# Optimization experiments

Measured on AMD Instinct MI355X. Metric: run time of the kernel, lower is better.

Reference implementation:

```python
import jax, jax.numpy as jnp
import numpy as np

HIDDEN = 256
TOPK = 16
SINK_BLOCKS = 5
TAU = 1.0
SOFT_ALPHA = 8.0
LN_EPS = 1e-5


def setup_inputs() -> dict:
    key = jax.random.key(0)
    ks = jax.random.split(key, 8)
    B, T, QD, KD, J = 2, 1024, 1024, 1024, 64
    H = HIDDEN
    H3 = 3 * H
    s = 0.02
    return {
        "Q": jax.random.normal(ks[0], (B, T, QD), dtype=jnp.float32),
        "K": jax.random.normal(ks[1], (B, J, KD), dtype=jnp.float32),
        "Wq": jax.random.normal(ks[2], (H, QD), dtype=jnp.float32) * s,
        "Wk": jax.random.normal(ks[3], (H, KD), dtype=jnp.float32) * s,
        "ln_g": jnp.ones((H3,), dtype=jnp.float32),
        "ln_b": jnp.zeros((H3,), dtype=jnp.float32),
        "Wu": jax.random.normal(ks[4], (H, H3), dtype=jnp.float32) * s,
        "bu": jnp.zeros((H,), dtype=jnp.float32),
        "Wv": jax.random.normal(ks[5], (H, H3), dtype=jnp.float32) * s,
        "bv": jnp.zeros((H,), dtype=jnp.float32),
        "Wo": jax.random.normal(ks[6], (1, H), dtype=jnp.float32) * s,
        "bo": jnp.zeros((1,), dtype=jnp.float32),
        "chunk_len": 16,
        "L_ctx": 1024,
    }


def _forward(Q, K, Wq, Wk, ln_g, ln_b, Wu, bu, Wv, bv, Wo, bo, chunk_len, L_ctx):
    B, T, _ = Q.shape
    J = K.shape[1]
    # ---- GatedScorer ----
    q = jnp.einsum('btd,hd->bth', Q, Wq)  # (B,T,H)
    k = jnp.einsum('bjd,hd->bjh', K, Wk)  # (B,J,H)
    H = q.shape[-1]
    qb = jnp.broadcast_to(q[:, :, None, :], (B, T, J, H))
    kb = jnp.broadcast_to(k[:, None, :, :], (B, T, J, H))
    x = jnp.concatenate([qb, kb, qb * kb], axis=-1)  # (B,T,J,3H)
    mu = jnp.mean(x, axis=-1, keepdims=True)
    var = jnp.mean((x - mu) ** 2, axis=-1, keepdims=True)
    x = (x - mu) / jnp.sqrt(var + LN_EPS) * ln_g + ln_b
    U = jnp.einsum('btjc,hc->btjh', x, Wu) + bu
    V = jnp.einsum('btjc,hc->btjh', x, Wv) + bv
    Z = U * jax.nn.gelu(V, approximate=False)
    logits = jnp.einsum('btjh,oh->btjo', Z, Wo)[..., 0] + bo[0]  # (B,T,J)

    # ---- top-k chunk selection (deterministic path, use_learnable_k=False) ----
    sink = int(min(max(0, SINK_BLOCKS), J))
    J_tail = J - sink
    topk_main = max(min(J, TOPK) - sink, 0)
    logits_tail = logits[..., sink:]  # (B,T,J_tail)
    causal = jnp.arange(J_tail)[None, :] <= jnp.arange(T)[:, None]  # tril(T,J_tail)
    masked = jnp.where(causal[None], logits_tail, -jnp.inf)
    _, idx_tail = jax.lax.top_k(masked, topk_main)
    idx_tail = idx_tail + sink
    sink_idx = jnp.broadcast_to(jnp.arange(sink)[None, None, :], (B, T, sink))
    idx = jnp.concatenate([sink_idx, idx_tail], axis=-1)  # (B,T,sink+topk_main)

    # ---- soft warmup weights ----
    w_soft = jax.nn.softmax(logits / TAU, axis=-1)  # (B,T,J)

    # ---- build_block_bias_from_topk ----
    num_chunks = (L_ctx + chunk_len - 1) // chunk_len
    sel = jnp.zeros((B, T, num_chunks), dtype=bool)
    sel = sel.at[jnp.arange(B)[:, None, None], jnp.arange(T)[None, :, None], idx].set(True)
    token_chunk = jnp.clip(jnp.arange(L_ctx) // chunk_len, 0, num_chunks - 1)  # (L_ctx,)
    sel_tok = jnp.take(sel, token_chunk, axis=-1)  # (B,T,L_ctx)
    per_chunk_bias = -SOFT_ALPHA * (1.0 - w_soft)  # (B,T,J)
    bias = jnp.take(per_chunk_bias, token_chunk, axis=-1)  # (B,T,L_ctx)
    bias = jnp.where(sel_tok, 0.0, bias)
    tri = jnp.arange(L_ctx)[None, :] > jnp.arange(T)[:, None]  # triu(T,L_ctx, diag=1)
    bias = jnp.where(tri[None], -jnp.inf, bias)
    return logits, bias


def reference(Q, K, Wq, Wk, ln_g, ln_b, Wu, bu, Wv, bv, Wo, bo, chunk_len, L_ctx):
    return _forward(Q, K, Wq, Wk, ln_g, ln_b, Wu, bu, Wv, bv, Wo, bo, chunk_len, L_ctx)
```

## Files before the change

kernel.cpp:

```cpp
#include <hip/hip_runtime.h>
#include <hip/hip_bf16.h>
#include <math.h>

#define H3 768

#define OFF_Q     0u
#define OFF_K     524288u
#define OFF_UVK   557056u
#define OFF_SQ    622592u
#define OFF_SQ2   624768u
#define OFF_WGU   626944u
#define OFF_WGV   627200u
#define OFF_CU    627456u
#define OFF_CV    627712u
#define OFF_Q2    627968u
#define OFF_K2    1152256u

#define BO_UVQ   0u
#define BO_WQF   1048576u
#define BO_WKF   1310720u
#define BO_BPK   1572864u
#define BO_WQBF  1703936u
#define BO_WKBF  1835008u

typedef __attribute__((ext_vector_type(8))) short bf16x8;
typedef __attribute__((ext_vector_type(4))) float f32x4;

__device__ __forceinline__ float bf2f(short s) {
    return __uint_as_float(((unsigned)(unsigned short)s) << 16);
}
union bfu { __hip_bfloat162 h; short2 s; };
__device__ __forceinline__ void split2(float a, float b, short* hi2, short* lo2) {
    bfu h; h.h = __float22bfloat162_rn(float2{a, b});
    float fa = bf2f(h.s.x), fb = bf2f(h.s.y);
    bfu l; l.h = __float22bfloat162_rn(float2{a - fa, b - fb});
    hi2[0] = h.s.x; hi2[1] = h.s.y;
    lo2[0] = l.s.x; lo2[1] = l.s.y;
}
__device__ __forceinline__ void split8(const float* v, bf16x8* vh, bf16x8* vl) {
    short h2[2], l2[2];
#pragma unroll
    for (int i = 0; i < 4; i++) {
        split2(v[2 * i], v[2 * i + 1], h2, l2);
        (*vh)[2 * i] = h2[0]; (*vh)[2 * i + 1] = h2[1];
        (*vl)[2 * i] = l2[0]; (*vl)[2 * i + 1] = l2[1];
    }
}

__device__ __forceinline__ float gelu_fast(float v) {
    float ar = v * 0.70710678118654752440f;
    float a = fabsf(ar);
    float t = __builtin_amdgcn_rcpf(fmaf(0.3275911f, a, 1.0f));
    float p = fmaf(fmaf(fmaf(fmaf(1.061405429f, t, -1.453152027f), t,
                             1.421413741f), t, -0.284496736f), t, 0.254829592f) * t;
    float e = __expf(-ar * ar);
    float er = fmaf(-p, e, 1.0f);
    er = copysignf(er, ar);
    return 0.5f * v * (1.0f + er);
}

__device__ __forceinline__ float wave_reduce_add(float v) {
#pragma unroll
    for (int off = 32; off > 0; off >>= 1) v += __shfl_xor(v, off, 64);
    return v;
}

__global__ __launch_bounds__(256) void prep(const float* __restrict__ Wq,
                                            const float* __restrict__ Wk,
                                            const float* __restrict__ Wu,
                                            const float* __restrict__ Wv,
                                            const float* __restrict__ g,
                                            const float* __restrict__ lb,
                                            const float* __restrict__ bu,
                                            const float* __restrict__ bv,
                                            float* __restrict__ ws,
                                            float* __restrict__ bsc) {
    int tid = threadIdx.x;
    int bid = blockIdx.x;
    if (bid < 64) {
        int h = bid * 4 + (tid >> 6);
        int lane = tid & 63;
        float su = 0.f, sv = 0.f, tu = 0.f, tv = 0.f;
#pragma unroll
        for (int i = 0; i < 12; i++) {
            int c = lane + 64 * i;
            float gg = g[c], bb = lb[c];
            float wu = Wu[h * H3 + c], wv = Wv[h * H3 + c];
            su += wu * gg; sv += wv * gg; tu += wu * bb; tv += wv * bb;
        }
        su = wave_reduce_add(su); sv = wave_reduce_add(sv);
        tu = wave_reduce_add(tu); tv = wave_reduce_add(tv);
        if (lane == 0) {
            ws[OFF_WGU + h] = su; ws[OFF_WGV + h] = sv;
            ws[OFF_CU + h] = tu + bu[h]; ws[OFF_CV + h] = tv + bv[h];
        }
        return;
    }
    float v8[8];
    bf16x8 vh, vl;
    if (bid < 320) {
        const float* W; bf16x8* dst;
        int idx;
        if (bid < 192) { idx = (bid - 64) * 256 + tid; W = Wq; dst = (bf16x8*)(bsc + BO_WQF); }
        else { idx = (bid - 192) * 256 + tid; W = Wk; dst = (bf16x8*)(bsc + BO_WKF); }
        int n = idx >> 7, k8 = idx & 127;
        const float* src = W + (size_t)n * 1024 + k8 * 8;
        *(float4*)&v8[0] = *(const float4*)src;
        *(float4*)&v8[4] = *(const float4*)(src + 4);
        split8(v8, &vh, &vl);
        int kc = k8 >> 2, grp = k8 & 3, lane = grp * 16 + (n & 15), ntg = n >> 4;
        size_t s0 = ((size_t)(kc * 16 + ntg) * 2) * 64 + lane;
        dst[s0] = vh; dst[s0 + 64] = vl;
        return;
    }
    int idx, c0;
    bf16x8* dst;
    int n;
    if (bid < 384) {
        idx = (bid - 320) * 256 + tid;
        n = idx >> 5; c0 = (idx & 31) * 8;
        dst = (bf16x8*)(bsc + BO_WQBF);
    } else if (bid < 448) {
        idx = (bid - 384) * 256 + tid;
        n = idx >> 5; c0 = 256 + (idx & 31) * 8;
        dst = (bf16x8*)(bsc + BO_WKBF);
    } else {
        idx = (bid - 448) * 256 + tid;
        n = idx >> 5; c0 = 512 + (idx & 31) * 8;
        dst = (bf16x8*)(bsc + BO_BPK);
    }
    int h, uv;
    if (bid < 448) { uv = (n < 256) ? 0 : 1; h = (n < 256) ? n : n - 256; }
    else {
        int ntg0 = n >> 4, cc = n & 15;
        uv = ntg0 & 1;
        h = ((ntg0 >> 3) << 6) | (((ntg0 >> 1) & 3) << 4) | cc;
    }
    const float* W = uv ? Wv : Wu;
#pragma unroll
    for (int i = 0; i < 8; i++) v8[i] = W[(size_t)h * H3 + c0 + i] * g[c0 + i];
    split8(v8, &vh, &vl);
    int k8 = (c0 & 255) >> 3;
    int kc = k8 >> 2, grp = k8 & 3, lane = grp * 16 + (n & 15), ntg = n >> 4;
    size_t s0 = ((size_t)(kc * 32 + ntg) * 2) * 64 + lane;
    dst[s0] = vh; dst[s0 + 64] = vl;
}

__global__ __launch_bounds__(256) void proj_mfma(const float* __restrict__ Q,
                                                 const float* __restrict__ Kin,
                                                 const float* __restrict__ bsc,
                                                 float* __restrict__ ws) {
    __shared__ __align__(16) short Ah[2][32 * 40], Al[2][32 * 40];
    int tid = threadIdx.x, bx = blockIdx.x, by = blockIdx.y, ks = blockIdx.z;
    const float* A; float* C; const bf16x8* BF;
    if (by < 64) {
        A = Q + (size_t)by * 32 * 1024;
        C = ws + (ks ? OFF_Q2 : OFF_Q) + (size_t)by * 32 * 256;
        BF = (const bf16x8*)(bsc + BO_WQF);
    } else {
        A = Kin + (size_t)(by - 64) * 32 * 1024;
        C = ws + (ks ? OFF_K2 : OFF_K) + (size_t)(by - 64) * 32 * 256;
        BF = (const bf16x8*)(bsc + BO_WKF);
    }
    int w = tid >> 6, l = tid & 63, c15 = l & 15, grp = l >> 4;
    int mt = w & 1, np = w >> 1;
    int srow = tid >> 3, scol = (tid & 7) * 4;
    const float* arow = A + (size_t)srow * 1024 + ks * 512 + scol;
    f32x4 acc[2];
    acc[0] = (f32x4){0.f, 0.f, 0.f, 0.f};
    acc[1] = (f32x4){0.f, 0.f, 0.f, 0.f};
    float4 a4 = *(const float4*)&arow[0];
    for (int kc = 0; kc < 16; kc++) {
        int pb = kc & 1;
        short h4[4], l4[4];
        split2(a4.x, a4.y, &h4[0], &l4[0]);
        split2(a4.z, a4.w, &h4[2], &l4[2]);
        int ao = srow * 40 + scol;
        *(short4*)&Ah[pb][ao] = *(short4*)&h4[0];
        *(short4*)&Al[pb][ao] = *(short4*)&l4[0];
        if (kc < 15) a4 = *(const float4*)&arow[(kc + 1) * 32];
        __syncthreads();
        int fo = (mt * 16 + c15) * 40 + grp * 8;
        bf16x8 afh = *(const bf16x8*)&Ah[pb][fo];
        bf16x8 afl = *(const bf16x8*)&Al[pb][fo];
        int kcg = ks * 16 + kc;
        bf16x8 bh[2], bl[2];
#pragma unroll
        for (int i = 0; i < 2; i++) {
            int ntg = bx * 4 + 2 * np + i;
            size_t fi = ((size_t)(kcg * 16 + ntg) * 2) * 64 + l;
            bh[i] = BF[fi]; bl[i] = BF[fi + 64];
        }
#pragma unroll
        for (int i = 0; i < 2; i++)
            acc[i] = __builtin_amdgcn_mfma_f32_16x16x32_bf16(afl, bh[i], acc[i], 0, 0, 0);
#pragma unroll
        for (int i = 0; i < 2; i++)
            acc[i] = __builtin_amdgcn_mfma_f32_16x16x32_bf16(afh, bl[i], acc[i], 0, 0, 0);
#pragma unroll
        for (int i = 0; i < 2; i++)
            acc[i] = __builtin_amdgcn_mfma_f32_16x16x32_bf16(afh, bh[i], acc[i], 0, 0, 0);
    }
#pragma unroll
    for (int r = 0; r < 4; r++) {
        int rloc = mt * 16 + grp * 4 + r;
#pragma unroll
        for (int i = 0; i < 2; i++)
            C[(size_t)rloc * 256 + bx * 64 + (2 * np + i) * 16 + c15] = acc[i][r];
    }
}

__global__ __launch_bounds__(256) void uv_mfma(float* __restrict__ ws,
                                               float* __restrict__ bsc) {
    __shared__ __align__(16) short Ah[64 * 40], Al[64 * 40];
    int tid = threadIdx.x, bx = blockIdx.x, by = blockIdx.y;
    const float* A1; const float* A2; float* C; const bf16x8* BF; int sbase;
    if (by < 32) {
        A1 = ws + OFF_Q + (size_t)by * 64 * 256;
        A2 = ws + OFF_Q2 + (size_t)by * 64 * 256;
        C = bsc + BO_UVQ + (size_t)by * 64 * 512;
        BF = (const bf16x8*)(bsc + BO_WQBF);
        sbase = by * 64;
    } else {
        A1 = ws + OFF_K + (size_t)(by - 32) * 64 * 256;
        A2 = ws + OFF_K2 + (size_t)(by - 32) * 64 * 256;
        C = ws + OFF_UVK + (size_t)(by - 32) * 64 * 512;
        BF = (const bf16x8*)(bsc + BO_WKBF);
        sbase = 2048 + (by - 32) * 64;
    }
    int w = tid >> 6, l = tid & 63, c15 = l & 15, grp = l >> 4;
    int srow = tid >> 2, scol = (tid & 3) * 8;
    f32x4 acc[4];
#pragma unroll
    for (int nt = 0; nt < 4; nt++) acc[nt] = (f32x4){0.f, 0.f, 0.f, 0.f};
    float s1 = 0.f, s2 = 0.f;
    for (int kc = 0; kc < 8; kc++) {
        float v8[8], u8[8];
        const float* src1 = &A1[(size_t)srow * 256 + kc * 32 + scol];
        const float* src2 = &A2[(size_t)srow * 256 + kc * 32 + scol];
        *(float4*)&v8[0] = *(const float4*)src1;
        *(float4*)&v8[4] = *(const float4*)(src1 + 4);
        *(float4*)&u8[0] = *(const float4*)src2;
        *(float4*)&u8[4] = *(const float4*)(src2 + 4);
#pragma unroll
        for (int i = 0; i < 8; i++) v8[i] += u8[i];
        if (bx == 0) {
#pragma unroll
            for (int i = 0; i < 8; i++) { s1 += v8[i]; s2 = fmaf(v8[i], v8[i], s2); }
        }
        bf16x8 vh, vl;
        split8(v8, &vh, &vl);
        int ao = srow * 40 + scol;
        *(bf16x8*)&Ah[ao] = vh;
        *(bf16x8*)&Al[ao] = vl;
        __syncthreads();
        int fo = (w * 16 + c15) * 40 + grp * 8;
        bf16x8 afh = *(const bf16x8*)&Ah[fo];
        bf16x8 afl = *(const bf16x8*)&Al[fo];
        bf16x8 bh[4], bl[4];
#pragma unroll
        for (int nt = 0; nt < 4; nt++) {
            int ntg = bx * 4 + nt;
            size_t fi = ((size_t)(kc * 32 + ntg) * 2) * 64 + l;
            bh[nt] = BF[fi]; bl[nt] = BF[fi + 64];
        }
#pragma unroll
        for (int nt = 0; nt < 4; nt++)
            acc[nt] = __builtin_amdgcn_mfma_f32_16x16x32_bf16(afl, bh[nt], acc[nt], 0, 0, 0);
#pragma unroll
        for (int nt = 0; nt < 4; nt++)
            acc[nt] = __builtin_amdgcn_mfma_f32_16x16x32_bf16(afh, bl[nt], acc[nt], 0, 0, 0);
#pragma unroll
        for (int nt = 0; nt < 4; nt++)
            acc[nt] = __builtin_amdgcn_mfma_f32_16x16x32_bf16(afh, bh[nt], acc[nt], 0, 0, 0);
        __syncthreads();
    }
    if (bx == 0) {
        s1 += __shfl_xor(s1, 1, 64); s1 += __shfl_xor(s1, 2, 64);
        s2 += __shfl_xor(s2, 1, 64); s2 += __shfl_xor(s2, 2, 64);
        if ((tid & 3) == 0) {
            ws[OFF_SQ + sbase + srow] = s1;
            ws[OFF_SQ2 + sbase + srow] = s2;
        }
    }
#pragma unroll
    for (int nt = 0; nt < 4; nt++)
#pragma unroll
        for (int r = 0; r < 4; r++)
            C[(size_t)(w * 16 + grp * 4 + r) * 512 + bx * 64 + nt * 16 + c15] = acc[nt][r];
}

__global__ __launch_bounds__(256, 2) void main_mfma(const float* __restrict__ ws,
                                                    const float* __restrict__ bsc,
                                                    const float* __restrict__ Wo,
                                                    const float* __restrict__ bo,
                                                    float* __restrict__ logits) {
    __shared__ float kk[256];
    __shared__ __align__(16) short Ah[8][64 * 32];
    __shared__ __align__(16) short Al[8][64 * 32];
    __shared__ float mu_s[64], inv_s[64];
    __shared__ float part_s[4][64];
    int tid = threadIdx.x;
    int bidf = blockIdx.x;
    int ti = ((bidf & 7) << 1) | ((bidf >> 3) & 1);
    int j = (bidf >> 4) & 63;
    int b = bidf >> 10;
    int t0 = ti << 6;
    int bj = (b << 6) | j;
    int rot8 = bidf & 7;
    kk[tid] = ws[OFF_K + bj * 256 + tid] + ws[OFF_K2 + bj * 256 + tid];
    int w = tid >> 6, l = tid & 63, c15 = l & 15, grp = l >> 4;
    int srow = tid >> 2, scol = (tid & 3) * 8;
    const float* qrow = ws + OFF_Q + (size_t)((b << 10) + t0 + srow) * 256 + scol;
    const float* q2row = ws + OFF_Q2 + (size_t)((b << 10) + t0 + srow) * 256 + scol;
    const bf16x8* bpk = (const bf16x8*)(bsc + BO_BPK);
    const float* UVQ = bsc + BO_UVQ;
    f32x4 acc[4][8];
#pragma unroll
    for (int mt = 0; mt < 4; mt++)
#pragma unroll
        for (int nt = 0; nt < 8; nt++) acc[mt][nt] = (f32x4){0.f, 0.f, 0.f, 0.f};
    float s1 = 0.f, s2 = 0.f;
    int ntg0 = w * 8;
    __syncthreads();
#pragma unroll
    for (int kc = 0; kc < 8; kc++) {
        float q8[8], p8[8], kv[8];
        *(float4*)&q8[0] = *(const float4*)&qrow[kc * 32];
        *(float4*)&q8[4] = *(const float4*)&qrow[kc * 32 + 4];
        *(float4*)&p8[0] = *(const float4*)&q2row[kc * 32];
        *(float4*)&p8[4] = *(const float4*)&q2row[kc * 32 + 4];
        *(float4*)&kv[0] = *(const float4*)&kk[kc * 32 + scol];
        *(float4*)&kv[4] = *(const float4*)&kk[kc * 32 + scol + 4];
        bf16x8 vh, vl;
        short htmp[2], ltmp[2];
#pragma unroll
        for (int i = 0; i < 4; i++) {
            float a = (q8[2 * i] + p8[2 * i]) * kv[2 * i];
            float c = (q8[2 * i + 1] + p8[2 * i + 1]) * kv[2 * i + 1];
            s1 += a + c;
            s2 = fmaf(a, a, s2); s2 = fmaf(c, c, s2);
            split2(a, c, htmp, ltmp);
            vh[2 * i] = htmp[0]; vh[2 * i + 1] = htmp[1];
            vl[2 * i] = ltmp[0]; vl[2 * i + 1] = ltmp[1];
        }
        int ao = srow * 32 + scol;
        *(bf16x8*)&Ah[kc][ao] = vh;
        *(bf16x8*)&Al[kc][ao] = vl;
    }
    s1 += __shfl_xor(s1, 1, 64); s1 += __shfl_xor(s1, 2, 64);
    s2 += __shfl_xor(s2, 1, 64); s2 += __shfl_xor(s2, 2, 64);
    if ((tid & 3) == 0) {
        int row = (b << 10) + t0 + srow;
        float sq = s1 + ws[OFF_SQ + row] + ws[OFF_SQ + 2048 + bj];
        float sq2 = s2 + ws[OFF_SQ2 + row] + ws[OFF_SQ2 + 2048 + bj];
        float muv = sq * (1.0f / 768.0f);
        float ex2 = sq2 * (1.0f / 768.0f);
        mu_s[srow] = muv;
        inv_s[srow] = 1.0f / sqrtf(ex2 - muv * muv + 1e-5f);
    }
    __syncthreads();
#pragma unroll
    for (int ii = 0; ii < 8; ii++) {
        int kcg = (ii + rot8) & 7;
        bf16x8 afh[4], afl[4];
#pragma unroll
        for (int mt = 0; mt < 4; mt++) {
            int ao = (mt * 16 + c15) * 32 + grp * 8;
            afh[mt] = *(const bf16x8*)&Ah[kcg][ao];
            afl[mt] = *(const bf16x8*)&Al[kcg][ao];
        }
        const bf16x8* bpc = bpk + ((size_t)(kcg * 32 + ntg0) * 2) * 64 + l;
#pragma unroll
        for (int nt = 0; nt < 8; nt++) {
            bf16x8 bh = bpc[(size_t)nt * 128];
            bf16x8 bl = bpc[(size_t)nt * 128 + 64];
#pragma unroll
            for (int mt = 0; mt < 4; mt++)
                acc[mt][nt] = __builtin_amdgcn_mfma_f32_16x16x32_bf16(afl[mt], bh, acc[mt][nt], 0, 0, 0);
#pragma unroll
            for (int mt = 0; mt < 4; mt++)
                acc[mt][nt] = __builtin_amdgcn_mfma_f32_16x16x32_bf16(afh[mt], bl, acc[mt][nt], 0, 0, 0);
#pragma unroll
            for (int mt = 0; mt < 4; mt++)
                acc[mt][nt] = __builtin_amdgcn_mfma_f32_16x16x32_bf16(afh[mt], bh, acc[mt][nt], 0, 0, 0);
        }
    }
    float wgu_r[4], wgv_r[4], cu_r[4], cv_r[4], wo_r[4], uk_r[4], vk_r[4];
    int h4[4];
#pragma unroll
    for (int a = 0; a < 4; a++) {
        int h = (w << 6) | (a << 4) | c15;
        h4[a] = h;
        wgu_r[a] = ws[OFF_WGU + h]; wgv_r[a] = ws[OFF_WGV + h];
        cu_r[a] = ws[OFF_CU + h]; cv_r[a] = ws[OFF_CV + h];
        wo_r[a] = Wo[h];
        uk_r[a] = ws[OFF_UVK + (size_t)bj * 512 + h];
        vk_r[a] = ws[OFF_UVK + (size_t)bj * 512 + 256 + h];
    }
#pragma unroll
    for (int mt = 0; mt < 4; mt++) {
#pragma unroll
        for (int r4 = 0; r4 < 4; r4++) {
            int r = mt * 16 + grp * 4 + r4;
            int row = (b << 10) + t0 + r;
            float muv = mu_s[r], invv = inv_s[r];
            const float* uvq = UVQ + (size_t)row * 512;
            float part = 0.f;
#pragma unroll
            for (int a = 0; a < 4; a++) {
                float U = invv * (acc[mt][2 * a][r4] + uvq[h4[a]] + uk_r[a] - muv * wgu_r[a]) + cu_r[a];
                float V = invv * (acc[mt][2 * a + 1][r4] + uvq[256 + h4[a]] + vk_r[a] - muv * wgv_r[a]) + cv_r[a];
                part = fmaf(wo_r[a] * U, gelu_fast(V), part);
            }
            part += __shfl_xor(part, 1, 64);
            part += __shfl_xor(part, 2, 64);
            part += __shfl_xor(part, 4, 64);
            part += __shfl_xor(part, 8, 64);
            if (c15 == 0) part_s[w][r] = part;
        }
    }
    __syncthreads();
    if (tid < 64) {
        float v = bo[0] + part_s[0][tid] + part_s[1][tid] + part_s[2][tid] + part_s[3][tid];
        logits[(size_t)((b << 10) + t0 + tid) * 64 + j] = v;
    }
}

__global__ __launch_bounds__(256) void topk_bias(const float* __restrict__ logits,
                                                 float* __restrict__ bias,
                                                 const int* __restrict__ p_cl,
                                                 const int* __restrict__ p_L) {
    int wv = threadIdx.x >> 6, lane = threadIdx.x & 63;
    int row = blockIdx.x * 4 + wv;
    int t = row & 1023;
    __shared__ float pcb[4][64];
    float L = logits[(size_t)row * 64 + lane];
    float mx = L;
#pragma unroll
    for (int off = 32; off > 0; off >>= 1) mx = fmaxf(mx, __shfl_xor(mx, off, 64));
    float e = expf(L - mx);
    float s = wave_reduce_add(e);
    pcb[wv][lane] = -8.0f * (1.0f - e / s);
    bool valid = (lane >= 5) && ((lane - 5) <= t);
    float val = (lane >= 5) ? (valid ? L : -INFINITY) : -INFINITY;
    int idv = (lane >= 5) ? lane : (1 << 28);
    unsigned long long selmask = 0x1Full;
    for (int it = 0; it < 11; it++) {
        float bv = val; int bi = idv;
#pragma unroll
        for (int off = 32; off > 0; off >>= 1) {
            float ov = __shfl_xor(bv, off, 64);
            int oi = __shfl_xor(bi, off, 64);
            if (ov > bv || (ov == bv && oi < bi)) { bv = ov; bi = oi; }
        }
        selmask |= 1ull << bi;
        if (lane == bi) { val = -INFINITY; idv = (1 << 27); }
    }
    int clen = p_cl[0], Lctx = p_L[0];
    int nch1 = (Lctx + clen - 1) / clen - 1;
    float* brow = bias + (size_t)row * Lctx;
    if ((Lctx & 3) == 0) {
        float4* brow4 = (float4*)brow;
        for (int q = lane; q < (Lctx >> 2); q += 64) {
            float o[4];
#pragma unroll
            for (int i = 0; i < 4; i++) {
                int ll = 4 * q + i;
                int c = min(min((unsigned)ll / (unsigned)clen, (unsigned)nch1), 63u);
                float v;
                if (ll > t) v = -1e30f;
                else if ((selmask >> c) & 1ull) v = 0.0f;
                else v = pcb[wv][c];
                o[i] = v;
            }
            brow4[q] = *(float4*)&o[0];
        }
    } else {
        for (int ll = lane; ll < Lctx; ll += 64) {
            int c = min(min((unsigned)ll / (unsigned)clen, (unsigned)nch1), 63u);
            float v;
            if (ll > t) v = -1e30f;
            else if ((selmask >> c) & 1ull) v = 0.0f;
            else v = pcb[wv][c];
            brow[ll] = v;
        }
    }
}

extern "C" void kernel_launch(void* const* d_in, const int* in_sizes, int n_in,
                              void* d_out, int out_size, void* d_ws, size_t ws_size,
                              hipStream_t stream) {
    const float* Q   = (const float*)d_in[0];
    const float* Kin = (const float*)d_in[1];
    const float* Wq  = (const float*)d_in[2];
    const float* Wk  = (const float*)d_in[3];
    const float* g   = (const float*)d_in[4];
    const float* lb  = (const float*)d_in[5];
    const float* Wu  = (const float*)d_in[6];
    const float* bu  = (const float*)d_in[7];
    const float* Wv  = (const float*)d_in[8];
    const float* bv  = (const float*)d_in[9];
    const float* Wo  = (const float*)d_in[10];
    const float* bo  = (const float*)d_in[11];
    const int* p_cl  = (const int*)d_in[12];
    const int* p_L   = (const int*)d_in[13];
    float* ws = (float*)d_ws;
    float* logits = (float*)d_out;
    float* bias = (float*)d_out + (size_t)2 * 1024 * 64;

    prep<<<512, 256, 0, stream>>>(Wq, Wk, Wu, Wv, g, lb, bu, bv, ws, bias);
    proj_mfma<<<dim3(4, 68, 2), 256, 0, stream>>>(Q, Kin, bias, ws);
    uv_mfma<<<dim3(8, 34), 256, 0, stream>>>(ws, bias);
    main_mfma<<<2048, 256, 0, stream>>>(ws, bias, Wo, bo, logits);
    topk_bias<<<512, 256, 0, stream>>>(logits, bias, p_cl, p_L);
}
```

Measured before the change: 234.1 us.

## Enlarge main_mfma tile to 128 rows with 512-thread blocks

```diff
diff --git a/kernel.cpp b/kernel.cpp
--- a/kernel.cpp
+++ b/kernel.cpp
@@ -290,38 +290,38 @@
             C[(size_t)(w * 16 + grp * 4 + r) * 512 + bx * 64 + nt * 16 + c15] = acc[nt][r];
 }
 
-__global__ __launch_bounds__(256, 2) void main_mfma(const float* __restrict__ ws,
+__global__ __launch_bounds__(512, 2) void main_mfma(const float* __restrict__ ws,
                                                     const float* __restrict__ bsc,
                                                     const float* __restrict__ Wo,
                                                     const float* __restrict__ bo,
                                                     float* __restrict__ logits) {
     __shared__ float kk[256];
-    __shared__ __align__(16) short Ah[8][64 * 32];
-    __shared__ __align__(16) short Al[8][64 * 32];
-    __shared__ float mu_s[64], inv_s[64];
-    __shared__ float part_s[4][64];
+    __shared__ __align__(16) short Ah[8][128 * 32];
+    __shared__ __align__(16) short Al[8][128 * 32];
+    __shared__ float mu_s[128], inv_s[128];
+    __shared__ float part_s[8][128];
     int tid = threadIdx.x;
     int bidf = blockIdx.x;
-    int ti = ((bidf & 7) << 1) | ((bidf >> 3) & 1);
-    int j = (bidf >> 4) & 63;
-    int b = bidf >> 10;
-    int t0 = ti << 6;
+    int ti = bidf & 7;
+    int j = (bidf >> 3) & 63;
+    int b = bidf >> 9;
+    int t0 = ti << 7;
     int bj = (b << 6) | j;
-    int rot8 = bidf & 7;
-    kk[tid] = ws[OFF_K + bj * 256 + tid] + ws[OFF_K2 + bj * 256 + tid];
+    int rot8 = (bidf >> 3) & 7;
+    if (tid < 256) kk[tid] = ws[OFF_K + bj * 256 + tid] + ws[OFF_K2 + bj * 256 + tid];
     int w = tid >> 6, l = tid & 63, c15 = l & 15, grp = l >> 4;
     int srow = tid >> 2, scol = (tid & 3) * 8;
     const float* qrow = ws + OFF_Q + (size_t)((b << 10) + t0 + srow) * 256 + scol;
     const float* q2row = ws + OFF_Q2 + (size_t)((b << 10) + t0 + srow) * 256 + scol;
     const bf16x8* bpk = (const bf16x8*)(bsc + BO_BPK);
     const float* UVQ = bsc + BO_UVQ;
-    f32x4 acc[4][8];
-#pragma unroll
-    for (int mt = 0; mt < 4; mt++)
-#pragma unroll
-        for (int nt = 0; nt < 8; nt++) acc[mt][nt] = (f32x4){0.f, 0.f, 0.f, 0.f};
+    f32x4 acc[8][4];
+#pragma unroll
+    for (int mt = 0; mt < 8; mt++)
+#pragma unroll
+        for (int nt = 0; nt < 4; nt++) acc[mt][nt] = (f32x4){0.f, 0.f, 0.f, 0.f};
     float s1 = 0.f, s2 = 0.f;
-    int ntg0 = w * 8;
+    int ntg0 = w * 4;
     __syncthreads();
 #pragma unroll
     for (int kc = 0; kc < 8; kc++) {
@@ -363,35 +363,43 @@
 #pragma unroll
     for (int ii = 0; ii < 8; ii++) {
         int kcg = (ii + rot8) & 7;
-        bf16x8 afh[4], afl[4];
-#pragma unroll
-        for (int mt = 0; mt < 4; mt++) {
-            int ao = (mt * 16 + c15) * 32 + grp * 8;
-            afh[mt] = *(const bf16x8*)&Ah[kcg][ao];
-            afl[mt] = *(const bf16x8*)&Al[kcg][ao];
-        }
+        bf16x8 bh[4], bl[4];
         const bf16x8* bpc = bpk + ((size_t)(kcg * 32 + ntg0) * 2) * 64 + l;
 #pragma unroll
-        for (int nt = 0; nt < 8; nt++) {
-            bf16x8 bh = bpc[(size_t)nt * 128];
-            bf16x8 bl = bpc[(size_t)nt * 128 + 64];
-#pragma unroll
-            for (int mt = 0; mt < 4; mt++)
-                acc[mt][nt] = __builtin_amdgcn_mfma_f32_16x16x32_bf16(afl[mt], bh, acc[mt][nt], 0, 0, 0);
-#pragma unroll
-            for (int mt = 0; mt < 4; mt++)
-                acc[mt][nt] = __builtin_amdgcn_mfma_f32_16x16x32_bf16(afh[mt], bl, acc[mt][nt], 0, 0, 0);
-#pragma unroll
-            for (int mt = 0; mt < 4; mt++)
-                acc[mt][nt] = __builtin_amdgcn_mfma_f32_16x16x32_bf16(afh[mt], bh, acc[mt][nt], 0, 0, 0);
-        }
-    }
-    float wgu_r[4], wgv_r[4], cu_r[4], cv_r[4], wo_r[4], uk_r[4], vk_r[4];
-    int h4[4];
-#pragma unroll
-    for (int a = 0; a < 4; a++) {
-        int h = (w << 6) | (a << 4) | c15;
-        h4[a] = h;
+        for (int nt = 0; nt < 4; nt++) {
+            bh[nt] = bpc[(size_t)nt * 128];
+            bl[nt] = bpc[(size_t)nt * 128 + 64];
+        }
+#pragma unroll
+        for (int half = 0; half < 2; half++) {
+            bf16x8 afh[4], afl[4];
+#pragma unroll
+            for (int m4 = 0; m4 < 4; m4++) {
+                int ao = ((half * 4 + m4) * 16 + c15) * 32 + grp * 8;
+                afh[m4] = *(const bf16x8*)&Ah[kcg][ao];
+                afl[m4] = *(const bf16x8*)&Al[kcg][ao];
+            }
+#pragma unroll
+            for (int nt = 0; nt < 4; nt++) {
+#pragma unroll
+                for (int m4 = 0; m4 < 4; m4++)
+                    acc[half * 4 + m4][nt] = __builtin_amdgcn_mfma_f32_16x16x32_bf16(afl[m4], bh[nt], acc[half * 4 + m4][nt], 0, 0, 0);
+#pragma unroll
+                for (int m4 = 0; m4 < 4; m4++)
+                    acc[half * 4 + m4][nt] = __builtin_amdgcn_mfma_f32_16x16x32_bf16(afh[m4], bl[nt], acc[half * 4 + m4][nt], 0, 0, 0);
+#pragma unroll
+                for (int m4 = 0; m4 < 4; m4++)
+                    acc[half * 4 + m4][nt] = __builtin_amdgcn_mfma_f32_16x16x32_bf16(afh[m4], bh[nt], acc[half * 4 + m4][nt], 0, 0, 0);
+            }
+        }
+    }
+    float wgu_r[2], wgv_r[2], cu_r[2], cv_r[2], wo_r[2], uk_r[2], vk_r[2];
+    int h2[2];
+#pragma unroll
+    for (int a = 0; a < 2; a++) {
+        int ntg = 4 * w + 2 * a;
+        int h = ((ntg >> 3) << 6) | (((ntg >> 1) & 3) << 4) | c15;
+        h2[a] = h;
         wgu_r[a] = ws[OFF_WGU + h]; wgv_r[a] = ws[OFF_WGV + h];
         cu_r[a] = ws[OFF_CU + h]; cv_r[a] = ws[OFF_CV + h];
         wo_r[a] = Wo[h];
@@ -399,7 +407,7 @@
         vk_r[a] = ws[OFF_UVK + (size_t)bj * 512 + 256 + h];
     }
 #pragma unroll
-    for (int mt = 0; mt < 4; mt++) {
+    for (int mt = 0; mt < 8; mt++) {
 #pragma unroll
         for (int r4 = 0; r4 < 4; r4++) {
             int r = mt * 16 + grp * 4 + r4;
@@ -408,9 +416,9 @@
             const float* uvq = UVQ + (size_t)row * 512;
             float part = 0.f;
 #pragma unroll
-            for (int a = 0; a < 4; a++) {
-                float U = invv * (acc[mt][2 * a][r4] + uvq[h4[a]] + uk_r[a] - muv * wgu_r[a]) + cu_r[a];
-                float V = invv * (acc[mt][2 * a + 1][r4] + uvq[256 + h4[a]] + vk_r[a] - muv * wgv_r[a]) + cv_r[a];
+            for (int a = 0; a < 2; a++) {
+                float U = invv * (acc[mt][2 * a][r4] + uvq[h2[a]] + uk_r[a] - muv * wgu_r[a]) + cu_r[a];
+                float V = invv * (acc[mt][2 * a + 1][r4] + uvq[256 + h2[a]] + vk_r[a] - muv * wgv_r[a]) + cv_r[a];
                 part = fmaf(wo_r[a] * U, gelu_fast(V), part);
             }
             part += __shfl_xor(part, 1, 64);
@@ -421,8 +429,10 @@
         }
     }
     __syncthreads();
-    if (tid < 64) {
-        float v = bo[0] + part_s[0][tid] + part_s[1][tid] + part_s[2][tid] + part_s[3][tid];
+    if (tid < 128) {
+        float v = bo[0];
+#pragma unroll
+        for (int ww = 0; ww < 8; ww++) v += part_s[ww][tid];
         logits[(size_t)((b << 10) + t0 + tid) * 64 + j] = v;
     }
 }
@@ -512,6 +522,6 @@
     prep<<<512, 256, 0, stream>>>(Wq, Wk, Wu, Wv, g, lb, bu, bv, ws, bias);
     proj_mfma<<<dim3(4, 68, 2), 256, 0, stream>>>(Q, Kin, bias, ws);
     uv_mfma<<<dim3(8, 34), 256, 0, stream>>>(ws, bias);
-    main_mfma<<<2048, 256, 0, stream>>>(ws, bias, Wo, bo, logits);
+    main_mfma<<<1024, 512, 0, stream>>>(ws, bias, Wo, bo, logits);
     topk_bias<<<512, 256, 0, stream>>>(logits, bias, p_cl, p_L);
 }
```

Measured after the change: 248.5 us. 6.2% more time.

## Merge split-K projection partials via atomics; use shift for pow2 chunk index

Applied to the files above, without the earlier changes.

```diff
diff --git a/kernel.cpp b/kernel.cpp
--- a/kernel.cpp
+++ b/kernel.cpp
@@ -13,8 +13,6 @@
 #define OFF_WGV   627200u
 #define OFF_CU    627456u
 #define OFF_CV    627712u
-#define OFF_Q2    627968u
-#define OFF_K2    1152256u
 
 #define BO_UVQ   0u
 #define BO_WQF   1048576u
@@ -77,6 +75,10 @@
                                             float* __restrict__ bsc) {
     int tid = threadIdx.x;
     int bid = blockIdx.x;
+    if (bid >= 512) {
+        ws[(bid - 512) * 256 + tid] = 0.0f;
+        return;
+    }
     if (bid < 64) {
         int h = bid * 4 + (tid >> 6);
         int lane = tid & 63;
@@ -155,11 +157,11 @@
     const float* A; float* C; const bf16x8* BF;
     if (by < 64) {
         A = Q + (size_t)by * 32 * 1024;
-        C = ws + (ks ? OFF_Q2 : OFF_Q) + (size_t)by * 32 * 256;
+        C = ws + OFF_Q + (size_t)by * 32 * 256;
         BF = (const bf16x8*)(bsc + BO_WQF);
     } else {
         A = Kin + (size_t)(by - 64) * 32 * 1024;
-        C = ws + (ks ? OFF_K2 : OFF_K) + (size_t)(by - 64) * 32 * 256;
+        C = ws + OFF_K + (size_t)(by - 64) * 32 * 256;
         BF = (const bf16x8*)(bsc + BO_WKF);
     }
     int w = tid >> 6, l = tid & 63, c15 = l & 15, grp = l >> 4;
@@ -206,7 +208,7 @@
         int rloc = mt * 16 + grp * 4 + r;
 #pragma unroll
         for (int i = 0; i < 2; i++)
-            C[(size_t)rloc * 256 + bx * 64 + (2 * np + i) * 16 + c15] = acc[i][r];
+            atomicAdd(&C[(size_t)rloc * 256 + bx * 64 + (2 * np + i) * 16 + c15], acc[i][r]);
     }
 }
 
@@ -214,16 +216,14 @@
                                                float* __restrict__ bsc) {
     __shared__ __align__(16) short Ah[64 * 40], Al[64 * 40];
     int tid = threadIdx.x, bx = blockIdx.x, by = blockIdx.y;
-    const float* A1; const float* A2; float* C; const bf16x8* BF; int sbase;
+    const float* A; float* C; const bf16x8* BF; int sbase;
     if (by < 32) {
-        A1 = ws + OFF_Q + (size_t)by * 64 * 256;
-        A2 = ws + OFF_Q2 + (size_t)by * 64 * 256;
+        A = ws + OFF_Q + (size_t)by * 64 * 256;
         C = bsc + BO_UVQ + (size_t)by * 64 * 512;
         BF = (const bf16x8*)(bsc + BO_WQBF);
         sbase = by * 64;
     } else {
-        A1 = ws + OFF_K + (size_t)(by - 32) * 64 * 256;
-        A2 = ws + OFF_K2 + (size_t)(by - 32) * 64 * 256;
+        A = ws + OFF_K + (size_t)(by - 32) * 64 * 256;
         C = ws + OFF_UVK + (size_t)(by - 32) * 64 * 512;
         BF = (const bf16x8*)(bsc + BO_WKBF);
         sbase = 2048 + (by - 32) * 64;
@@ -235,15 +235,10 @@
     for (int nt = 0; nt < 4; nt++) acc[nt] = (f32x4){0.f, 0.f, 0.f, 0.f};
     float s1 = 0.f, s2 = 0.f;
     for (int kc = 0; kc < 8; kc++) {
-        float v8[8], u8[8];
-        const float* src1 = &A1[(size_t)srow * 256 + kc * 32 + scol];
-        const float* src2 = &A2[(size_t)srow * 256 + kc * 32 + scol];
-        *(float4*)&v8[0] = *(const float4*)src1;
-        *(float4*)&v8[4] = *(const float4*)(src1 + 4);
-        *(float4*)&u8[0] = *(const float4*)src2;
-        *(float4*)&u8[4] = *(const float4*)(src2 + 4);
-#pragma unroll
-        for (int i = 0; i < 8; i++) v8[i] += u8[i];
+        float v8[8];
+        const float* src = &A[(size_t)srow * 256 + kc * 32 + scol];
+        *(float4*)&v8[0] = *(const float4*)src;
+        *(float4*)&v8[4] = *(const float4*)(src + 4);
         if (bx == 0) {
 #pragma unroll
             for (int i = 0; i < 8; i++) { s1 += v8[i]; s2 = fmaf(v8[i], v8[i], s2); }
@@ -308,11 +303,10 @@
     int t0 = ti << 6;
     int bj = (b << 6) | j;
     int rot8 = bidf & 7;
-    kk[tid] = ws[OFF_K + bj * 256 + tid] + ws[OFF_K2 + bj * 256 + tid];
+    kk[tid] = ws[OFF_K + bj * 256 + tid];
     int w = tid >> 6, l = tid & 63, c15 = l & 15, grp = l >> 4;
     int srow = tid >> 2, scol = (tid & 3) * 8;
     const float* qrow = ws + OFF_Q + (size_t)((b << 10) + t0 + srow) * 256 + scol;
-    const float* q2row = ws + OFF_Q2 + (size_t)((b << 10) + t0 + srow) * 256 + scol;
     const bf16x8* bpk = (const bf16x8*)(bsc + BO_BPK);
     const float* UVQ = bsc + BO_UVQ;
     f32x4 acc[4][8];
@@ -325,19 +319,17 @@
     __syncthreads();
 #pragma unroll
     for (int kc = 0; kc < 8; kc++) {
-        float q8[8], p8[8], kv[8];
+        float q8[8], kv[8];
         *(float4*)&q8[0] = *(const float4*)&qrow[kc * 32];
         *(float4*)&q8[4] = *(const float4*)&qrow[kc * 32 + 4];
-        *(float4*)&p8[0] = *(const float4*)&q2row[kc * 32];
-        *(float4*)&p8[4] = *(const float4*)&q2row[kc * 32 + 4];
         *(float4*)&kv[0] = *(const float4*)&kk[kc * 32 + scol];
         *(float4*)&kv[4] = *(const float4*)&kk[kc * 32 + scol + 4];
         bf16x8 vh, vl;
         short htmp[2], ltmp[2];
 #pragma unroll
         for (int i = 0; i < 4; i++) {
-            float a = (q8[2 * i] + p8[2 * i]) * kv[2 * i];
-            float c = (q8[2 * i + 1] + p8[2 * i + 1]) * kv[2 * i + 1];
+            float a = q8[2 * i] * kv[2 * i];
+            float c = q8[2 * i + 1] * kv[2 * i + 1];
             s1 += a + c;
             s2 = fmaf(a, a, s2); s2 = fmaf(c, c, s2);
             split2(a, c, htmp, ltmp);
@@ -459,6 +451,8 @@
     }
     int clen = p_cl[0], Lctx = p_L[0];
     int nch1 = (Lctx + clen - 1) / clen - 1;
+    bool p2 = (clen & (clen - 1)) == 0;
+    int sh = 31 - __clz(clen);
     float* brow = bias + (size_t)row * Lctx;
     if ((Lctx & 3) == 0) {
         float4* brow4 = (float4*)brow;
@@ -467,7 +461,8 @@
 #pragma unroll
             for (int i = 0; i < 4; i++) {
                 int ll = 4 * q + i;
-                int c = min(min((unsigned)ll / (unsigned)clen, (unsigned)nch1), 63u);
+                unsigned cq = p2 ? ((unsigned)ll >> sh) : ((unsigned)ll / (unsigned)clen);
+                int c = min(min(cq, (unsigned)nch1), 63u);
                 float v;
                 if (ll > t) v = -1e30f;
                 else if ((selmask >> c) & 1ull) v = 0.0f;
@@ -478,7 +473,8 @@
         }
     } else {
         for (int ll = lane; ll < Lctx; ll += 64) {
-            int c = min(min((unsigned)ll / (unsigned)clen, (unsigned)nch1), 63u);
+            unsigned cq = p2 ? ((unsigned)ll >> sh) : ((unsigned)ll / (unsigned)clen);
+            int c = min(min(cq, (unsigned)nch1), 63u);
             float v;
             if (ll > t) v = -1e30f;
             else if ((selmask >> c) & 1ull) v = 0.0f;
@@ -509,7 +505,7 @@
     float* logits = (float*)d_out;
     float* bias = (float*)d_out + (size_t)2 * 1024 * 64;
 
-    prep<<<512, 256, 0, stream>>>(Wq, Wk, Wu, Wv, g, lb, bu, bv, ws, bias);
+    prep<<<2688, 256, 0, stream>>>(Wq, Wk, Wu, Wv, g, lb, bu, bv, ws, bias);
     proj_mfma<<<dim3(4, 68, 2), 256, 0, stream>>>(Q, Kin, bias, ws);
     uv_mfma<<<dim3(8, 34), 256, 0, stream>>>(ws, bias);
     main_mfma<<<2048, 256, 0, stream>>>(ws, bias, Wo, bo, logits);
```

Measured after the change: 232.3 us. About the same (-0.8%).
